# Kernel optimization log

Hardware: AMD Instinct MI355X
Metric: run time of the kernel (lower is better)

Reference implementation:

```python
import jax, jax.numpy as jnp
import numpy as np

DIM = 1024; DEPTH = 2; HEADS = 8; DH = DIM // HEADS  # 128
BUCKET = 64; NHASH = 4; MULT = 4
B = 2; T = 4096
NBUCKETS = T // BUCKET  # 64
SCALE = DH ** -0.5
SELF_ATTN_VAL = -5e4  # TOKEN_SELF_ATTN_VALUE in reformer-pytorch
EPS = 1e-5


def layer_norm(x, g, b):
    m = jnp.mean(x, -1, keepdims=True)
    v = jnp.var(x, -1, keepdims=True)
    return (x - m) * jax.lax.rsqrt(v + EPS) * g + b


def lsh_attn(xn, Wqk, Wv, Wo, bo, rot):
    # xn: [B,T,DIM] already layer-normed. Shared-QK LSH attention (reformer-pytorch).
    qk = (xn @ Wqk).reshape(B, T, HEADS, DH).transpose(0, 2, 1, 3).reshape(B * HEADS, T, DH)
    v = (xn @ Wv).reshape(B, T, HEADS, DH).transpose(0, 2, 1, 3).reshape(B * HEADS, T, DH)
    bh = B * HEADS
    # --- hashing with random rotations ---
    rotated = jnp.einsum('btf,fhi->bhti', qk, rot)            # [bh,NHASH,T,NBUCKETS//2]
    rotated = jnp.concatenate([rotated, -rotated], -1)        # [bh,NHASH,T,NBUCKETS]
    buckets = jnp.argmax(rotated, -1)                         # [bh,NHASH,T]
    offs = (jnp.arange(NHASH) * NBUCKETS)[:, None]
    buckets = (buckets + offs).reshape(bh, NHASH * T)
    ticker = jnp.arange(NHASH * T)
    bt = buckets * T + (ticker % T)                           # unique keys -> stable-equivalent sort
    sticker = jnp.argsort(bt, axis=-1)                        # [bh, NHASH*T]
    undo = jnp.argsort(sticker, axis=-1)
    st = sticker % T                                          # original positions, bucket-sorted
    sqk = jnp.take_along_axis(qk, st[..., None], axis=1)
    sv = jnp.take_along_axis(v, st[..., None], axis=1)
    nchunks = NHASH * NBUCKETS
    bq_t = st.reshape(bh, nchunks, BUCKET)
    bqk = sqk.reshape(bh, nchunks, BUCKET, DH)
    bv = sv.reshape(bh, nchunks, BUCKET, DH)
    bq = bqk
    bk = bqk / jnp.clip(jnp.linalg.norm(bqk, axis=-1, keepdims=True), 1e-12)
    def look_one_back(a):
        extra = jnp.concatenate([a[:, -1:], a[:, :-1]], axis=1)
        return jnp.concatenate([a, extra], axis=2)
    bk = look_one_back(bk); bv = look_one_back(bv); bkv_t = look_one_back(bq_t)
    dots = jnp.einsum('bcie,bcje->bcij', bq, bk) * SCALE      # [bh,nchunks,BUCKET,2*BUCKET]
    self_mask = bq_t[..., :, None] == bkv_t[..., None, :]     # shared-QK: penalize i==j
    dots = jnp.where(self_mask, SELF_ATTN_VAL, dots)
    lse = jax.nn.logsumexp(dots, axis=-1, keepdims=True)
    p = jnp.exp(dots - lse)
    bo_ = jnp.einsum('bcij,bcje->bcie', p, bv)
    so = bo_.reshape(bh, NHASH * T, DH)
    slog = lse.reshape(bh, NHASH * T)
    o = jnp.take_along_axis(so, undo[..., None], axis=1)
    logits = jnp.take_along_axis(slog, undo, axis=1)
    o = o.reshape(bh, NHASH, T, DH)
    logits = logits.reshape(bh, NHASH, T, 1)
    probs = jnp.exp(logits - jax.nn.logsumexp(logits, axis=1, keepdims=True))
    out = jnp.sum(o * probs, axis=1)                          # combine hash rounds
    out = out.reshape(B, HEADS, T, DH).transpose(0, 2, 1, 3).reshape(B, T, HEADS * DH)
    return out @ Wo + bo


def setup_inputs() -> dict:
    key = jax.random.key(0)
    ks = jax.random.split(key, 16)
    s = 0.02
    d = {
        'x': jax.random.normal(ks[0], (B, T, DIM), jnp.float32),
        'ln1_g': jnp.ones((DEPTH, DIM), jnp.float32),
        'ln1_b': jnp.zeros((DEPTH, DIM), jnp.float32),
        'Wqk': jax.random.normal(ks[1], (DEPTH, DIM, HEADS * DH), jnp.float32) * s,
        'Wv': jax.random.normal(ks[2], (DEPTH, DIM, HEADS * DH), jnp.float32) * s,
        'Wo': jax.random.normal(ks[3], (DEPTH, HEADS * DH, DIM), jnp.float32) * s,
        'bo': jnp.zeros((DEPTH, DIM), jnp.float32),
        'ln2_g': jnp.ones((DEPTH, DIM), jnp.float32),
        'ln2_b': jnp.zeros((DEPTH, DIM), jnp.float32),
        'W1': jax.random.normal(ks[4], (DEPTH, DIM, DIM * MULT), jnp.float32) * s,
        'b1': jnp.zeros((DEPTH, DIM * MULT), jnp.float32),
        'W2': jax.random.normal(ks[5], (DEPTH, DIM * MULT, DIM), jnp.float32) * s,
        'b2': jnp.zeros((DEPTH, DIM), jnp.float32),
        'rotations': jax.random.normal(ks[6], (DEPTH, DH, NHASH, NBUCKETS // 2), jnp.float32),
    }
    return d


def reference(x, ln1_g, ln1_b, Wqk, Wv, Wo, bo, ln2_g, ln2_b, W1, b1, W2, b2, rotations):
    xx = jnp.concatenate([x, x], -1)  # [B,T,2*DIM] reversible pair
    def step(carry, p):
        g1, be1, wqk, wv, wo, bov, g2, be2, w1, bb1, w2, bb2, rot = p
        x1, x2 = jnp.split(carry, 2, axis=-1)
        y1 = x1 + lsh_attn(layer_norm(x2, g1, be1), wqk, wv, wo, bov, rot)
        h = layer_norm(y1, g2, be2)
        ff = jax.nn.gelu(h @ w1 + bb1, approximate=False) @ w2 + bb2
        y2 = x2 + ff
        return jnp.concatenate([y1, y2], -1), None
    params = (ln1_g, ln1_b, Wqk, Wv, Wo, bo, ln2_g, ln2_b, W1, b1, W2, b2, rotations)
    out, _ = jax.lax.scan(step, xx, params)
    y1, y2 = jnp.split(out, 2, axis=-1)
    return y1 + y2
```

## Files before the change

### kernel.cpp

```cpp
#include <hip/hip_runtime.h>
#include <hip/hip_bf16.h>
#include <cmath>

using bf16 = __hip_bfloat16;
typedef __attribute__((ext_vector_type(8))) short short8;
typedef __attribute__((ext_vector_type(4))) float floatx4;

__device__ __forceinline__ float bu2f(ushort u) { return __uint_as_float((unsigned)u << 16); }
__device__ __forceinline__ ushort f2bu(float f) {
  union { bf16 b; ushort u; } cv; cv.b = __float2bfloat16(f); return cv.u;
}
__device__ __forceinline__ void gl_lds16(const ushort* g, ushort* l) {
  __builtin_amdgcn_global_load_lds((const __attribute__((address_space(1))) unsigned*)g,
                                   (__attribute__((address_space(3))) unsigned*)l, 16, 0, 0);
}
__device__ __forceinline__ float fast_gelu(float x) {
  float z = 0.7978845608028654f * (x + 0.044715f * x * x * x);
  z = fmaxf(fminf(z, 10.f), -10.f);
  float e = __expf(2.f * z);
  float t = (e - 1.f) / (e + 1.f);
  return 0.5f * x * (1.f + t);
}

static constexpr int kT   = 4096;
static constexpr int kDim = 1024;
static constexpr float kScale   = 0.08838834764831845f;
static constexpr float kSelfVal = -5.0e4f;

__device__ __forceinline__ int sane_v(float f) { float a = fabsf(f); return (a > 1e-4f && a < 1e4f) ? 1 : 0; }

__global__ __launch_bounds__(256) void k_detect(const unsigned* __restrict__ x, int* __restrict__ flag) {
  __shared__ int cnt;
  int tid = threadIdx.x;
  if (tid == 0) cnt = 0;
  __syncthreads();
  int my = 0;
  const uint4* p = (const uint4*)x;
  for (int q = 0; q < 16; q++) {
    uint4 u = p[tid * 16 + q];
    my += sane_v(__uint_as_float(u.x << 16)) + sane_v(__uint_as_float(u.x & 0xffff0000u));
    my += sane_v(__uint_as_float(u.y << 16)) + sane_v(__uint_as_float(u.y & 0xffff0000u));
    my += sane_v(__uint_as_float(u.z << 16)) + sane_v(__uint_as_float(u.z & 0xffff0000u));
    my += sane_v(__uint_as_float(u.w << 16)) + sane_v(__uint_as_float(u.w & 0xffff0000u));
  }
  atomicAdd(&cnt, my);
  __syncthreads();
  if (tid == 0) flag[0] = (cnt >= 24576) ? 1 : 0;
}

__global__ __launch_bounds__(256) void k_cvt(const int* __restrict__ flag, const void* __restrict__ src,
                                             ushort* __restrict__ dst, int n) {
  int i = blockIdx.x * 256 + threadIdx.x;
  if (i >= n) return;
  dst[i] = (*flag) ? ((const ushort*)src)[i] : f2bu(((const float*)src)[i]);
}

__global__ __launch_bounds__(256) void k_init_any(const int* __restrict__ flag, const void* __restrict__ x,
                                                  float* __restrict__ x1, float* __restrict__ x2) {
  int i = blockIdx.x * 1024 + threadIdx.x * 4;
  float4 f;
  if (*flag) {
    ushort4 u = *(const ushort4*)((const ushort*)x + i);
    f.x = bu2f(u.x); f.y = bu2f(u.y); f.z = bu2f(u.z); f.w = bu2f(u.w);
  } else {
    f = *(const float4*)((const float*)x + i);
  }
  *(float4*)(x1 + i) = f;
  *(float4*)(x2 + i) = f;
}

__global__ __launch_bounds__(256) void k_final_any(const int* __restrict__ flag, const float* __restrict__ x1,
                                                   const float* __restrict__ x2, void* __restrict__ out) {
  int i = blockIdx.x * 1024 + threadIdx.x * 4;
  float4 a = *(const float4*)(x1 + i);
  float4 b = *(const float4*)(x2 + i);
  float4 s; s.x = a.x + b.x; s.y = a.y + b.y; s.z = a.z + b.z; s.w = a.w + b.w;
  if (*flag) {
    ushort4 u; u.x = f2bu(s.x); u.y = f2bu(s.y); u.z = f2bu(s.z); u.w = f2bu(s.w);
    *(ushort4*)((ushort*)out + i) = u;
  } else {
    *(float4*)((float*)out + i) = s;
  }
}

__global__ __launch_bounds__(256) void k_ln(const float* __restrict__ x, const ushort* __restrict__ g,
                                            const ushort* __restrict__ be, ushort* __restrict__ out) {
  __shared__ float ws[4], ws2[4];
  int row = blockIdx.x, tid = threadIdx.x;
  const float* xr = x + (size_t)row * kDim + tid * 4;
  float4 v = *(const float4*)xr;
  float s  = v.x + v.y + v.z + v.w;
  float s2 = v.x*v.x + v.y*v.y + v.z*v.z + v.w*v.w;
  #pragma unroll
  for (int off = 32; off; off >>= 1) { s += __shfl_down(s, off); s2 += __shfl_down(s2, off); }
  int wave = tid >> 6, lane = tid & 63;
  if (lane == 0) { ws[wave] = s; ws2[wave] = s2; }
  __syncthreads();
  s  = ws[0] + ws[1] + ws[2] + ws[3];
  s2 = ws2[0] + ws2[1] + ws2[2] + ws2[3];
  float mean = s * (1.f/1024.f);
  float var  = fmaxf(s2 * (1.f/1024.f) - mean*mean, 0.f);
  float rstd = rsqrtf(var + 1e-5f);
  int cb = tid * 4;
  ushort* o = out + (size_t)row * kDim + cb;
  o[0] = f2bu((v.x - mean) * rstd * bu2f(g[cb+0]) + bu2f(be[cb+0]));
  o[1] = f2bu((v.y - mean) * rstd * bu2f(g[cb+1]) + bu2f(be[cb+1]));
  o[2] = f2bu((v.z - mean) * rstd * bu2f(g[cb+2]) + bu2f(be[cb+2]));
  o[3] = f2bu((v.w - mean) * rstd * bu2f(g[cb+3]) + bu2f(be[cb+3]));
}

__global__ __launch_bounds__(256) void k_transpose2(const int* __restrict__ flag, const void* __restrict__ src_bf,
                                                    const void* __restrict__ src_f, ushort* __restrict__ out,
                                                    int K, int N) {
  __shared__ ushort tile[32][33];
  int isbf = *flag;
  int nb = blockIdx.x * 32, kb = blockIdx.y * 32;
  int tx = threadIdx.x & 31, ty = threadIdx.x >> 5;
  for (int r = ty; r < 32; r += 8) {
    size_t idx = (size_t)(kb + r) * N + nb + tx;
    tile[r][tx] = isbf ? ((const ushort*)src_bf)[idx] : f2bu(((const float*)src_f)[idx]);
  }
  __syncthreads();
  for (int r = ty; r < 32; r += 8) out[(size_t)(nb + r) * K + kb + tx] = tile[tx][r];
}

__global__ __launch_bounds__(256) void k_rot_t(const ushort* __restrict__ rot, ushort* __restrict__ rotT) {
  int tid = threadIdx.x;
  for (int idx = tid; idx < 16384; idx += 256) {
    int n = idx >> 7, k = idx & 127;
    rotT[idx] = rot[k * 128 + n];
  }
}

template <int MW>
__global__ __launch_bounds__(512, 2) void k_gemm2(const ushort* __restrict__ A, const ushort* __restrict__ Bt,
                                                  const ushort* __restrict__ bias, float* __restrict__ Cf,
                                                  ushort* __restrict__ Cb, ushort* __restrict__ Cb2,
                                                  int M, int N, int K, int mode) {
  constexpr int BM  = MW * 32;
  constexpr int LA  = MW / 4;
  constexpr int AHI = (MW == 8) ? 4 : 2;
  __shared__ alignas(16) ushort SAu[4 * BM * 32];
  __shared__ alignas(16) ushort SBu[4 * 256 * 32];

  const int tid  = threadIdx.x;
  const int lane = tid & 63, wave = tid >> 6;
  const int lr = lane & 15, g = lane >> 4;
  const int wm = wave >> 2, wn = wave & 3;

  const int nbx = gridDim.x;
  const int nwg = nbx * gridDim.y;
  const int bid = blockIdx.y * nbx + blockIdx.x;
  const int swz = (bid & 7) * (nwg >> 3) + (bid >> 3);
  const int m0 = (swz / nbx) * BM;
  const int n0 = (swz % nbx) * 256;

  const int NT = K >> 5;

  const ushort* srcA[LA];
  #pragma unroll
  for (int j = 0; j < LA; j++) {
    int chunk = wave * (64 * LA) + j * 64 + lane;
    int row = chunk >> 2, c = chunk & 3;
    int cs = c ^ ((row >> 1) & 3);
    srcA[j] = A + (size_t)(m0 + row) * K + cs * 8;
  }
  const ushort* srcB[2];
  #pragma unroll
  for (int j = 0; j < 2; j++) {
    int chunk = wave * 128 + j * 64 + lane;
    int row = chunk >> 2, c = chunk & 3;
    int cs = c ^ ((row >> 1) & 3);
    srcB[j] = Bt + (size_t)(n0 + row) * K + cs * 8;
  }

  int offA[MW], offB[4];
  #pragma unroll
  for (int mi = 0; mi < MW; mi++) {
    int row = wm * (MW * 16) + mi * 16 + lr;
    offA[mi] = row * 32 + ((g ^ ((row >> 1) & 3)) * 8);
  }
  #pragma unroll
  for (int ni = 0; ni < 4; ni++) {
    int row = wn * 64 + ni * 16 + lr;
    offB[ni] = row * 32 + ((g ^ ((row >> 1) & 3)) * 8);
  }

  floatx4 acc[MW][4];
  #pragma unroll
  for (int mi = 0; mi < MW; mi++)
    #pragma unroll
    for (int ni = 0; ni < 4; ni++) acc[mi][ni] = (floatx4){0.f, 0.f, 0.f, 0.f};

  #pragma unroll
  for (int p = 0; p < 3; p++) {
    #pragma unroll
    for (int j = 0; j < LA; j++) gl_lds16(srcA[j] + p * 32, SAu + p * (BM * 32) + (wave * (64 * LA) + j * 64) * 8);
    #pragma unroll
    for (int j = 0; j < 2; j++)  gl_lds16(srcB[j] + p * 32, SBu + p * (256 * 32) + (wave * 128 + j * 64) * 8);
  }
  if constexpr (MW == 8) asm volatile("s_waitcnt vmcnt(8)" ::: "memory");
  else                   asm volatile("s_waitcnt vmcnt(6)" ::: "memory");
  __builtin_amdgcn_s_barrier();
  asm volatile("" ::: "memory");

  for (int kt = 0; kt < NT; kt++) {
    const ushort* sa = SAu + (kt & 3) * (BM * 32);
    const ushort* sb = SBu + (kt & 3) * (256 * 32);
    const bool pf = (kt + 3 < NT);
    const int kp = (kt + 3) * 32, pb = (kt + 3) & 3;

    short8 aA[AHI], bb[4];
    #pragma unroll
    for (int i = 0; i < AHI; i++) aA[i] = *(const short8*)&sa[offA[i]];
    #pragma unroll
    for (int ni = 0; ni < 4; ni++) bb[ni] = *(const short8*)&sb[offB[ni]];
    if (pf) {
      if constexpr (MW == 8) {
        gl_lds16(srcA[0] + kp, SAu + pb * (BM * 32) + (wave * 128 + 0) * 8);
        gl_lds16(srcA[1] + kp, SAu + pb * (BM * 32) + (wave * 128 + 64) * 8);
      } else {
        gl_lds16(srcA[0] + kp, SAu + pb * (BM * 32) + (wave * 64) * 8);
        gl_lds16(srcB[0] + kp, SBu + pb * (256 * 32) + (wave * 128 + 0) * 8);
      }
    }
    __builtin_amdgcn_s_barrier();
    __builtin_amdgcn_sched_barrier(0);
    __builtin_amdgcn_s_setprio(1);
    #pragma unroll
    for (int mi = 0; mi < AHI; mi++)
      #pragma unroll
      for (int ni = 0; ni < 4; ni++)
        acc[mi][ni] = __builtin_amdgcn_mfma_f32_16x16x32_bf16(aA[mi], bb[ni], acc[mi][ni], 0, 0, 0);
    __builtin_amdgcn_s_setprio(0);
    __builtin_amdgcn_sched_barrier(0);
    __builtin_amdgcn_s_barrier();
    asm volatile("" ::: "memory");

    short8 aB[MW - AHI];
    #pragma unroll
    for (int i = 0; i < MW - AHI; i++) aB[i] = *(const short8*)&sa[offA[AHI + i]];
    if (pf) {
      if constexpr (MW == 8) {
        gl_lds16(srcB[0] + kp, SBu + pb * (256 * 32) + (wave * 128 + 0) * 8);
        gl_lds16(srcB[1] + kp, SBu + pb * (256 * 32) + (wave * 128 + 64) * 8);
      } else {
        gl_lds16(srcB[1] + kp, SBu + pb * (256 * 32) + (wave * 128 + 64) * 8);
      }
    }
    if (kt + 3 < NT) {
      if constexpr (MW == 8) asm volatile("s_waitcnt vmcnt(8)" ::: "memory");
      else                   asm volatile("s_waitcnt vmcnt(6)" ::: "memory");
    } else if (kt + 2 < NT) {
      if constexpr (MW == 8) asm volatile("s_waitcnt vmcnt(4)" ::: "memory");
      else                   asm volatile("s_waitcnt vmcnt(3)" ::: "memory");
    } else if (kt + 1 < NT) {
      asm volatile("s_waitcnt vmcnt(0)" ::: "memory");
    }
    __builtin_amdgcn_s_barrier();
    __builtin_amdgcn_sched_barrier(0);
    __builtin_amdgcn_s_setprio(1);
    #pragma unroll
    for (int mi = 0; mi < MW - AHI; mi++)
      #pragma unroll
      for (int ni = 0; ni < 4; ni++)
        acc[AHI + mi][ni] = __builtin_amdgcn_mfma_f32_16x16x32_bf16(aB[mi], bb[ni], acc[AHI + mi][ni], 0, 0, 0);
    __builtin_amdgcn_s_setprio(0);
    __builtin_amdgcn_sched_barrier(0);
    __builtin_amdgcn_s_barrier();
    asm volatile("" ::: "memory");
  }

  const int hi4 = (lane >> 4) * 4;

  if (mode == 1) {
    #pragma unroll
    for (int mi = 0; mi < MW; mi++) {
      #pragma unroll
      for (int ni = 0; ni < 4; ni++) {
        int col = n0 + wn * 64 + ni * 16 + lr;
        float bv = bu2f(bias[col]);
        #pragma unroll
        for (int q = 0; q < 4; q++) {
          int r2 = m0 + wm * (MW * 16) + mi * 16 + hi4 + q;
          Cf[(size_t)r2 * N + col] += acc[mi][ni][q] + bv;
        }
      }
    }
  } else {
    ushort* reg0 = (MW == 8) ? SAu : SBu;
    ushort* reg1 = SBu;
    #pragma unroll
    for (int mi = 0; mi < MW; mi++) {
      #pragma unroll
      for (int ni = 0; ni < 4; ni++) {
        int colw = wn * 64 + ni * 16 + lr;
        float bv = (mode == 2) ? bu2f(bias[n0 + colw]) : 0.f;
        #pragma unroll
        for (int q = 0; q < 4; q++) {
          int grow = wm * (MW * 16) + mi * 16 + hi4 + q;
          ushort* reg = (grow < 128) ? reg0 : reg1;
          int rl = grow & 127;
          float val = acc[mi][ni][q];
          ushort h = (mode == 2) ? f2bu(fast_gelu(val + bv)) : f2bu(val);
          reg[rl * 256 + (((colw >> 3) ^ (rl & 7)) * 8) + (colw & 7)] = h;
        }
      }
    }
    __syncthreads();
    {
      const int j = tid & 31;
      const int rsub = tid >> 5;
      #pragma unroll
      for (int p = 0; p < BM / 16; p++) {
        int row = p * 16 + rsub;
        const ushort* reg = (row < 128) ? reg0 : reg1;
        int rl = row & 127;
        short8 v = *(const short8*)&reg[rl * 256 + ((j ^ (rl & 7)) * 8)];
        *(short8*)&Cb[(size_t)(m0 + row) * N + n0 + j * 8] = v;
      }
    }
    if (mode == 5) {
      __syncthreads();
      #pragma unroll
      for (int mi = 0; mi < MW; mi++) {
        #pragma unroll
        for (int ni = 0; ni < 4; ni++) {
          int colw = wn * 64 + ni * 16 + lr;
          #pragma unroll
          for (int q = 0; q < 4; q++) {
            int grow = wm * (MW * 16) + mi * 16 + hi4 + q;
            ushort* reg = (grow < 128) ? reg0 : reg1;
            int rl = grow & 127;
            float val = acc[mi][ni][q];
            ushort h = f2bu(val);
            reg[rl * 256 + (((colw >> 3) ^ (rl & 7)) * 8) + (colw & 7)] = f2bu(val - bu2f(h));
          }
        }
      }
      __syncthreads();
      const int j = tid & 31;
      const int rsub = tid >> 5;
      #pragma unroll
      for (int p = 0; p < BM / 16; p++) {
        int row = p * 16 + rsub;
        const ushort* reg = (row < 128) ? reg0 : reg1;
        int rl = row & 127;
        short8 v = *(const short8*)&reg[rl * 256 + ((j ^ (rl & 7)) * 8)];
        *(short8*)&Cb2[(size_t)(m0 + row) * N + n0 + j * 8] = v;
      }
    }
  }
  (void)M;
}

__global__ __launch_bounds__(512, 2) void k_gemm3(const ushort* __restrict__ A, const ushort* __restrict__ Bt,
                                                  const ushort* __restrict__ bias, ushort* __restrict__ Cb,
                                                  int M, int N, int K) {
  __shared__ alignas(16) ushort SA[2 * 256 * 64];
  __shared__ alignas(16) ushort SB[2 * 256 * 64];
  const int tid  = threadIdx.x;
  const int lane = tid & 63, wave = tid >> 6;
  const int lr = lane & 15, g = lane >> 4;
  const int wm = wave >> 2, wn = wave & 3;

  const int nbx = gridDim.x;
  const int nwg = nbx * gridDim.y;
  const int bid = blockIdx.y * nbx + blockIdx.x;
  const int swz = (bid & 7) * (nwg >> 3) + (bid >> 3);
  const int m0 = (swz / nbx) * 256;
  const int n0 = (swz % nbx) * 256;
  const int NT = K >> 6;
  const int NI = NT >> 1;

  const int chAr = (wave * 64 + lane) >> 3;
  const int chAs = (wave * 64 + lane) & 7;
  const int swA  = (chAs ^ (chAr & 7)) * 8;
  const ushort* sAq[2][2];
  #pragma unroll
  for (int q = 0; q < 2; q++)
    #pragma unroll
    for (int j = 0; j < 2; j++)
      sAq[q][j] = A + (size_t)(m0 + q * 64 + j * 128 + chAr) * K + swA;
  const int chBr = lane >> 3;
  const int swB  = ((lane & 7) ^ chBr) * 8;
  const ushort* sBh[2][2];
  #pragma unroll
  for (int h = 0; h < 2; h++)
    #pragma unroll
    for (int j = 0; j < 2; j++)
      sBh[h][j] = Bt + (size_t)(n0 + h * 128 + wave * 16 + j * 8 + chBr) * K + swB;

  int rA[8], rB[4], cK[2];
  #pragma unroll
  for (int mi = 0; mi < 8; mi++) rA[mi] = (wm * 128 + mi * 16 + lr) * 64;
  #pragma unroll
  for (int ni = 0; ni < 4; ni++) rB[ni] = (wn * 64 + ni * 16 + lr) * 64;
  cK[0] = ((0 * 4 + g) ^ (lr & 7)) * 8;
  cK[1] = ((1 * 4 + g) ^ (lr & 7)) * 8;

  floatx4 acc[8][4];
  #pragma unroll
  for (int mi = 0; mi < 8; mi++)
    #pragma unroll
    for (int ni = 0; ni < 4; ni++) acc[mi][ni] = (floatx4){0.f, 0.f, 0.f, 0.f};

#define G3_STG_A(d, q, kt) { int ko = ((kt) < NT ? (kt) : 0) << 6; \
    gl_lds16(sAq[q][0] + ko, SA + (d) * 16384 + ((q) * 64 + wave * 8) * 64); \
    gl_lds16(sAq[q][1] + ko, SA + (d) * 16384 + (128 + (q) * 64 + wave * 8) * 64); }
#define G3_STG_B(d, h, kt) { int ko = ((kt) < NT ? (kt) : 0) << 6; \
    gl_lds16(sBh[h][0] + ko, SB + (d) * 16384 + ((h) * 128 + wave * 16) * 64); \
    gl_lds16(sBh[h][1] + ko, SB + (d) * 16384 + ((h) * 128 + wave * 16 + 8) * 64); }
#define G3_RD_A(dst, d, kk, mb) { _Pragma("unroll") \
    for (int _m = 0; _m < 4; _m++) dst[_m] = *(const short8*)&SA[(d) * 16384 + rA[(mb) + _m] + cK[kk]]; }
#define G3_RD_B(dst, d, kk) { _Pragma("unroll") \
    for (int _n = 0; _n < 4; _n++) dst[_n] = *(const short8*)&SB[(d) * 16384 + rB[_n] + cK[kk]]; }
#define G3_MM(mb, af, bf) { \
    __builtin_amdgcn_s_setprio(1); \
    _Pragma("unroll") for (int _m = 0; _m < 4; _m++) \
      _Pragma("unroll") for (int _n = 0; _n < 4; _n++) \
        acc[(mb) + _m][_n] = __builtin_amdgcn_mfma_f32_16x16x32_bf16(af[_m], bf[_n], acc[(mb) + _m][_n], 0, 0, 0); \
    __builtin_amdgcn_s_setprio(0); }
#define G3_BAR()  __builtin_amdgcn_s_barrier()
#define G3_SB()   __builtin_amdgcn_sched_barrier(0)

  G3_STG_A(0, 0, 0); G3_STG_A(0, 1, 0); G3_STG_B(0, 0, 0); G3_STG_B(0, 1, 0);
  G3_STG_A(1, 0, 1); G3_STG_B(1, 0, 1);
  asm volatile("s_waitcnt vmcnt(4)" ::: "memory");
  G3_BAR();
  asm volatile("" ::: "memory");

  for (int i = 0; i < NI; i++) {
    const int kb = 2 * i;
    short8 aA[4], bb0[4], bb1[4];
    G3_RD_A(aA, 0, 0, 0); G3_RD_B(bb0, 0, 0); G3_STG_B(1, 1, kb + 1);
    G3_BAR(); G3_SB();
    G3_MM(0, aA, bb0);
    G3_SB(); G3_BAR(); asm volatile("" ::: "memory");
    G3_RD_A(aA, 0, 1, 0); G3_RD_B(bb1, 0, 1); G3_STG_A(1, 1, kb + 1);
    G3_BAR(); G3_SB();
    G3_MM(0, aA, bb1);
    G3_SB(); G3_BAR(); asm volatile("" ::: "memory");
    G3_RD_A(aA, 0, 0, 4); G3_STG_A(0, 0, kb + 2);
    G3_BAR(); G3_SB();
    G3_MM(4, aA, bb0);
    G3_SB(); G3_BAR(); asm volatile("" ::: "memory");
    G3_RD_A(aA, 0, 1, 4); G3_STG_B(0, 0, kb + 2);
    G3_BAR(); G3_SB();
    G3_MM(4, aA, bb1);
    G3_SB();
    asm volatile("s_waitcnt vmcnt(6)" ::: "memory");
    G3_BAR(); asm volatile("" ::: "memory");
    G3_RD_A(aA, 1, 0, 0); G3_RD_B(bb0, 1, 0); G3_STG_B(0, 1, kb + 2);
    G3_BAR(); G3_SB();
    G3_MM(0, aA, bb0);
    G3_SB(); G3_BAR(); asm volatile("" ::: "memory");
    G3_RD_A(aA, 1, 1, 0); G3_RD_B(bb1, 1, 1); G3_STG_A(0, 1, kb + 2);
    G3_BAR(); G3_SB();
    G3_MM(0, aA, bb1);
    G3_SB();
    asm volatile("s_waitcnt vmcnt(8)" ::: "memory");
    G3_BAR(); asm volatile("" ::: "memory");
    G3_RD_A(aA, 1, 0, 4); G3_STG_A(1, 0, kb + 3);
    G3_BAR(); G3_SB();
    G3_MM(4, aA, bb0);
    G3_SB(); G3_BAR(); asm volatile("" ::: "memory");
    G3_RD_A(aA, 1, 1, 4); G3_STG_B(1, 0, kb + 3);
    G3_BAR(); G3_SB();
    G3_MM(4, aA, bb1);
    G3_SB();
    asm volatile("s_waitcnt vmcnt(4)" ::: "memory");
    G3_BAR(); asm volatile("" ::: "memory");
  }

  asm volatile("s_waitcnt vmcnt(0)" ::: "memory");
  __syncthreads();

  const int hi4 = (lane >> 4) * 4;
  ushort* reg0 = SA;
  ushort* reg1 = SB;
  #pragma unroll
  for (int mi = 0; mi < 8; mi++) {
    #pragma unroll
    for (int ni = 0; ni < 4; ni++) {
      int colw = wn * 64 + ni * 16 + lr;
      float bv = bu2f(bias[n0 + colw]);
      #pragma unroll
      for (int q = 0; q < 4; q++) {
        int grow = wm * 128 + mi * 16 + hi4 + q;
        ushort* reg = (grow < 128) ? reg0 : reg1;
        int rl = grow & 127;
        reg[rl * 256 + (((colw >> 3) ^ (rl & 7)) * 8) + (colw & 7)] = f2bu(fast_gelu(acc[mi][ni][q] + bv));
      }
    }
  }
  __syncthreads();
  {
    const int j = tid & 31;
    const int rsub = tid >> 5;
    #pragma unroll
    for (int p = 0; p < 16; p++) {
      int row = p * 16 + rsub;
      const ushort* reg = (row < 128) ? reg0 : reg1;
      int rl = row & 127;
      short8 v = *(const short8*)&reg[rl * 256 + ((j ^ (rl & 7)) * 8)];
      *(short8*)&Cb[(size_t)(m0 + row) * N + n0 + j * 8] = v;
    }
  }
  (void)M;
#undef G3_STG_A
#undef G3_STG_B
#undef G3_RD_A
#undef G3_RD_B
#undef G3_MM
#undef G3_BAR
#undef G3_SB
}

__global__ __launch_bounds__(256) void k_bucket_mfma(const ushort* __restrict__ qkh, const ushort* __restrict__ qkl,
                                                     const ushort* __restrict__ rotT, int* __restrict__ bkt) {
  __shared__ alignas(16) ushort Bs[128*128];
  __shared__ alignas(16) ushort Ah[64*128];
  __shared__ alignas(16) ushort Al[64*128];
  const int tid = threadIdx.x;
  const int lane = tid & 63, wave = tid >> 6;
  const int lr = lane & 15, lk = (lane >> 4) * 8;
  const int tt = blockIdx.x * 64;
  const int bh = blockIdx.y;
  const int b = bh >> 3, hh = bh & 7;

  {
    int r = tid >> 2, c0 = (tid & 3) * 32;
    size_t base = ((size_t)(b * kT + tt + r)) * kDim + hh * 128 + c0;
    const uint4* sh = (const uint4*)(qkh + base);
    const uint4* sl = (const uint4*)(qkl + base);
    uint4* dh = (uint4*)&Ah[r * 128 + c0];
    uint4* dl = (uint4*)&Al[r * 128 + c0];
    #pragma unroll
    for (int i = 0; i < 4; i++) { dh[i] = sh[i]; dl[i] = sl[i]; }
  }
  {
    const uint4* src = (const uint4*)rotT;
    uint4* dst = (uint4*)Bs;
    for (int i = tid; i < 2048; i += 256) dst[i] = src[i];
  }
  __syncthreads();

  floatx4 acc[4][2];
  #pragma unroll
  for (int mi = 0; mi < 4; mi++) { acc[mi][0] = (floatx4){0,0,0,0}; acc[mi][1] = (floatx4){0,0,0,0}; }
  #pragma unroll
  for (int ks = 0; ks < 4; ks++) {
    short8 a[4], bb[2];
    #pragma unroll
    for (int ni = 0; ni < 2; ni++) bb[ni] = *(const short8*)&Bs[(wave*32 + ni*16 + lr)*128 + ks*32 + lk];
    #pragma unroll
    for (int mi = 0; mi < 4; mi++) a[mi] = *(const short8*)&Ah[(mi*16 + lr)*128 + ks*32 + lk];
    #pragma unroll
    for (int mi = 0; mi < 4; mi++)
      #pragma unroll
      for (int ni = 0; ni < 2; ni++)
        acc[mi][ni] = __builtin_amdgcn_mfma_f32_16x16x32_bf16(a[mi], bb[ni], acc[mi][ni], 0, 0, 0);
  }
  #pragma unroll
  for (int ks = 0; ks < 4; ks++) {
    short8 a[4], bb[2];
    #pragma unroll
    for (int ni = 0; ni < 2; ni++) bb[ni] = *(const short8*)&Bs[(wave*32 + ni*16 + lr)*128 + ks*32 + lk];
    #pragma unroll
    for (int mi = 0; mi < 4; mi++) a[mi] = *(const short8*)&Al[(mi*16 + lr)*128 + ks*32 + lk];
    #pragma unroll
    for (int mi = 0; mi < 4; mi++)
      #pragma unroll
      for (int ni = 0; ni < 2; ni++)
        acc[mi][ni] = __builtin_amdgcn_mfma_f32_16x16x32_bf16(a[mi], bb[ni], acc[mi][ni], 0, 0, 0);
  }

  #pragma unroll
  for (int mi = 0; mi < 4; mi++) {
    #pragma unroll
    for (int q = 0; q < 4; q++) {
      float v0 = acc[mi][0][q];
      float v1 = acc[mi][1][q];
      float best = v0; int bidx = lr;
      if (v1  > best) { best = v1;  bidx = 16 + lr; }
      if (-v0 > best) { best = -v0; bidx = 32 + lr; }
      if (-v1 > best) { best = -v1; bidx = 48 + lr; }
      #pragma unroll
      for (int m = 1; m <= 8; m <<= 1) {
        float ov = __shfl_xor(best, m);
        int   oi = __shfl_xor(bidx, m);
        if (ov > best || (ov == best && oi < bidx)) { best = ov; bidx = oi; }
      }
      if (lr == 0) {
        int row = mi*16 + ((lane >> 4) & 3)*4 + q;
        bkt[(bh*4 + wave)*4096 + tt + row] = bidx;
      }
    }
  }
}

__global__ __launch_bounds__(256) void k_sort(const int* __restrict__ bkt, int* __restrict__ st) {
  __shared__ unsigned char  hist[64*256];
  __shared__ unsigned short offs[64*256];
  __shared__ int base[64];
  int tid = threadIdx.x, grp = blockIdx.x;
  const int* bk = bkt + grp * 4096;
  for (int i = tid; i < 64*256; i += 256) hist[i] = 0;
  __syncthreads();
  int myb[16];
  #pragma unroll
  for (int j = 0; j < 16; j++) {
    myb[j] = bk[tid*16 + j];
    hist[myb[j]*256 + tid] += 1;
  }
  __syncthreads();
  if (tid < 64) {
    int run = 0;
    for (int t = 0; t < 256; t++) { offs[tid*256 + t] = (unsigned short)run; run += hist[tid*256 + t]; }
    base[tid] = run;
  }
  __syncthreads();
  if (tid == 0) {
    int run = 0;
    for (int b2 = 0; b2 < 64; b2++) { int c = base[b2]; base[b2] = run; run += c; }
  }
  __syncthreads();
  #pragma unroll
  for (int j = 0; j < 16; j++) {
    int b2 = myb[j];
    int r = 0;
    for (int jj = 0; jj < j; jj++) r += (myb[jj] == b2) ? 1 : 0;
    st[grp*4096 + base[b2] + (int)offs[b2*256 + tid] + r] = tid*16 + j;
  }
}

__global__ __launch_bounds__(256) void k_attn(const ushort* __restrict__ qkh, const ushort* __restrict__ vbuf,
                                              const int* __restrict__ st, ushort* __restrict__ o_r,
                                              float* __restrict__ lse_r) {
  __shared__ alignas(16) ushort KV[128*136];
  __shared__ alignas(16) ushort Ps[64*136];
  __shared__ float rnorm[128];
  __shared__ int   kposs[128];
  __shared__ float red1[64*4];
  __shared__ float red2[64*4];
  __shared__ float lrow[64];

  const int tid = threadIdx.x;
  const int bid = blockIdx.x;
  const int bh = bid >> 8;
  const int c  = bid & 255;
  const int h  = c >> 6;
  const int cprev = (c + 255) & 255;
  const int b  = bh >> 3, hh = bh & 7;
  const int lane = tid & 63, wave = tid >> 6;
  const int lr = lane & 15, lk = (lane >> 4) * 8;

  {
    int j = tid >> 1, half = tid & 1;
    int slot = (j < 64) ? (c*64 + j) : (cprev*64 + (j - 64));
    int pos = st[bh*16384 + slot];
    if (half == 0) kposs[j] = pos;
    const ushort* src = qkh + ((size_t)(b * kT + pos)) * kDim + hh*128 + half*64;
    float ss = 0.f;
    #pragma unroll
    for (int i2 = 0; i2 < 64; i2 += 8) {
      uint4 u = *(const uint4*)(src + i2);
      *(uint4*)&KV[j*136 + half*64 + i2] = u;
      float f0 = bu2f((ushort)(u.x & 0xffffu)), f1 = bu2f((ushort)(u.x >> 16));
      float f2 = bu2f((ushort)(u.y & 0xffffu)), f3 = bu2f((ushort)(u.y >> 16));
      float f4 = bu2f((ushort)(u.z & 0xffffu)), f5 = bu2f((ushort)(u.z >> 16));
      float f6 = bu2f((ushort)(u.w & 0xffffu)), f7 = bu2f((ushort)(u.w >> 16));
      ss += f0*f0 + f1*f1 + f2*f2 + f3*f3 + f4*f4 + f5*f5 + f6*f6 + f7*f7;
    }
    ss += __shfl_xor(ss, 1);
    if (half == 0) rnorm[j] = 1.f / fmaxf(sqrtf(ss), 1e-12f);
  }
  __syncthreads();

  {
    floatx4 acc[4][2];
    #pragma unroll
    for (int mi = 0; mi < 4; mi++) { acc[mi][0] = (floatx4){0,0,0,0}; acc[mi][1] = (floatx4){0,0,0,0}; }
    #pragma unroll
    for (int ks = 0; ks < 4; ks++) {
      short8 a[4], bb[2];
      #pragma unroll
      for (int mi = 0; mi < 4; mi++) a[mi]  = *(const short8*)&KV[(mi*16 + lr)*136 + ks*32 + lk];
      #pragma unroll
      for (int ni = 0; ni < 2; ni++) bb[ni] = *(const short8*)&KV[(wave*32 + ni*16 + lr)*136 + ks*32 + lk];
      #pragma unroll
      for (int mi = 0; mi < 4; mi++)
        #pragma unroll
        for (int ni = 0; ni < 2; ni++)
          acc[mi][ni] = __builtin_amdgcn_mfma_f32_16x16x32_bf16(a[mi], bb[ni], acc[mi][ni], 0, 0, 0);
    }
    #pragma unroll
    for (int mi = 0; mi < 4; mi++) {
      #pragma unroll
      for (int ni = 0; ni < 2; ni++) {
        int col = wave*32 + ni*16 + lr;
        float rn = rnorm[col] * kScale;
        int cpos = kposs[col];
        #pragma unroll
        for (int q = 0; q < 4; q++) {
          int row = mi*16 + (lane >> 4)*4 + q;
          float val = acc[mi][ni][q] * rn;
          if (cpos == kposs[row]) val = kSelfVal;
          Ps[row*136 + col] = f2bu(val);
        }
      }
    }
  }
  __syncthreads();

  {
    int j = tid >> 1, half = tid & 1;
    int pos = kposs[j];
    const ushort* src = vbuf + ((size_t)(b * kT + pos)) * kDim + hh*128 + half*64;
    #pragma unroll
    for (int i2 = 0; i2 < 64; i2 += 8) {
      uint4 u = *(const uint4*)(src + i2);
      int d0 = half*64 + i2;
      KV[(d0+0)*136 + j] = (ushort)(u.x & 0xffffu); KV[(d0+1)*136 + j] = (ushort)(u.x >> 16);
      KV[(d0+2)*136 + j] = (ushort)(u.y & 0xffffu); KV[(d0+3)*136 + j] = (ushort)(u.y >> 16);
      KV[(d0+4)*136 + j] = (ushort)(u.z & 0xffffu); KV[(d0+5)*136 + j] = (ushort)(u.z >> 16);
      KV[(d0+6)*136 + j] = (ushort)(u.w & 0xffffu); KV[(d0+7)*136 + j] = (ushort)(u.w >> 16);
    }
  }

  {
    int i = tid >> 2, part = tid & 3;
    const int jb = part * 32;
    float m = -1e30f;
    for (int j2 = 0; j2 < 32; j2++) m = fmaxf(m, bu2f(Ps[i*136 + jb + j2]));
    red1[i*4 + part] = m;
    __syncthreads();
    m = fmaxf(fmaxf(red1[i*4+0], red1[i*4+1]), fmaxf(red1[i*4+2], red1[i*4+3]));
    float ssum = 0.f;
    for (int j2 = 0; j2 < 32; j2++) {
      float arg = fmaxf(fminf(bu2f(Ps[i*136 + jb + j2]) - m, 0.f), -80.f);
      float p = __expf(arg);
      ssum += p;
      Ps[i*136 + jb + j2] = f2bu(p);
    }
    red2[i*4 + part] = ssum;
    __syncthreads();
    if (part == 0) {
      float l = fmaxf(red2[i*4+0] + red2[i*4+1] + red2[i*4+2] + red2[i*4+3], 1e-20f);
      lrow[i] = 1.f / l;
      lse_r[(size_t)(bh*4 + h)*4096 + kposs[i]] = m + __logf(l);
    }
  }
  __syncthreads();

  {
    floatx4 acc[4][2];
    #pragma unroll
    for (int mi = 0; mi < 4; mi++) { acc[mi][0] = (floatx4){0,0,0,0}; acc[mi][1] = (floatx4){0,0,0,0}; }
    #pragma unroll
    for (int ks = 0; ks < 4; ks++) {
      short8 a[4], bb[2];
      #pragma unroll
      for (int mi = 0; mi < 4; mi++) a[mi]  = *(const short8*)&Ps[(mi*16 + lr)*136 + ks*32 + lk];
      #pragma unroll
      for (int ni = 0; ni < 2; ni++) bb[ni] = *(const short8*)&KV[(wave*32 + ni*16 + lr)*136 + ks*32 + lk];
      #pragma unroll
      for (int mi = 0; mi < 4; mi++)
        #pragma unroll
        for (int ni = 0; ni < 2; ni++)
          acc[mi][ni] = __builtin_amdgcn_mfma_f32_16x16x32_bf16(a[mi], bb[ni], acc[mi][ni], 0, 0, 0);
    }
    #pragma unroll
    for (int mi = 0; mi < 4; mi++) {
      #pragma unroll
      for (int ni = 0; ni < 2; ni++) {
        int d = wave*32 + ni*16 + lr;
        #pragma unroll
        for (int q = 0; q < 4; q++) {
          int row = mi*16 + (lane >> 4)*4 + q;
          float o = acc[mi][ni][q] * lrow[row];
          o_r[((size_t)(bh*4 + h)*4096 + kposs[row])*128 + d] = f2bu(o);
        }
      }
    }
  }
}

__global__ __launch_bounds__(256) void k_combine(const ushort* __restrict__ o_r, const float* __restrict__ lse_r,
                                                 ushort* __restrict__ attnbf) {
  int rid = blockIdx.x * 2 + (threadIdx.x >> 7);
  int d = threadIdx.x & 127;
  int bh = rid >> 12, t = rid & 4095;
  int b = bh >> 3, hh = bh & 7;
  size_t base = (size_t)bh * 16384 + t;
  float l0 = lse_r[base], l1 = lse_r[base + 4096], l2 = lse_r[base + 8192], l3 = lse_r[base + 12288];
  float M = fmaxf(fmaxf(l0, l1), fmaxf(l2, l3));
  float e0 = __expf(fmaxf(fminf(l0 - M, 0.f), -80.f));
  float e1 = __expf(fmaxf(fminf(l1 - M, 0.f), -80.f));
  float e2 = __expf(fmaxf(fminf(l2 - M, 0.f), -80.f));
  float e3 = __expf(fmaxf(fminf(l3 - M, 0.f), -80.f));
  float inv = 1.f / (e0 + e1 + e2 + e3);
  float o = e0 * bu2f(o_r[(base         )*128 + d]) + e1 * bu2f(o_r[(base +  4096)*128 + d])
          + e2 * bu2f(o_r[(base +  8192)*128 + d]) + e3 * bu2f(o_r[(base + 12288)*128 + d]);
  attnbf[((size_t)b * kT + t) * kDim + hh*128 + d] = f2bu(o * inv);
}

extern "C" void kernel_launch(void* const* d_in, const int* in_sizes, int n_in,
                              void* d_out, int out_size, void* d_ws, size_t ws_size,
                              hipStream_t stream) {
  (void)in_sizes; (void)n_in; (void)out_size; (void)ws_size;
  const void* x     = d_in[0];
  const void* ln1_g = d_in[1];
  const void* ln1_b = d_in[2];
  const void* Wqk   = d_in[3];
  const void* Wv    = d_in[4];
  const void* Wo    = d_in[5];
  const void* bo    = d_in[6];
  const void* ln2_g = d_in[7];
  const void* ln2_b = d_in[8];
  const void* W1    = d_in[9];
  const void* b1    = d_in[10];
  const void* W2    = d_in[11];
  const void* b2    = d_in[12];
  const void* rot   = d_in[13];

  char* w = (char*)d_ws;
  int*    flag = (int*)w;    w += 256;
  ushort* prm  = (ushort*)w; w += 131072;
  float* x1  = (float*)w;  w += 33554432;
  float* x2  = (float*)w;  w += 33554432;
  ushort* qkh = (ushort*)w; w += 16777216;
  ushort* qkl = (ushort*)w; w += 16777216;
  ushort* vbb = (ushort*)w; w += 16777216;
  ushort* xbf = (ushort*)w; w += 16777216;
  ushort* orb = (ushort*)w; w += 67108864;
  float* lse = (float*)w;  w += 1048576;
  int*   bkt = (int*)w;    w += 1048576;
  int*   stb = (int*)w;    w += 1048576;
  ushort* wtA = (ushort*)w; w += 2097152;
  ushort* wtB = (ushort*)w; w += 2097152;
  ushort* wtC = (ushort*)w; w += 2097152;
  ushort* wt1 = (ushort*)w; w += 8388608;
  ushort* wt2 = (ushort*)w; w += 8388608;
  ushort* rtT = (ushort*)w; w += 32768;

  ushort* pLN1G = prm + 0;     ushort* pLN1B = prm + 2048;
  ushort* pBO   = prm + 4096;  ushort* pLN2G = prm + 6144;
  ushort* pLN2B = prm + 8192;  ushort* pB1   = prm + 10240;
  ushort* pB2   = prm + 18432; ushort* pROT  = prm + 20480;

  k_detect<<<1, 256, 0, stream>>>((const unsigned*)x, flag);
  k_cvt<<<8,   256, 0, stream>>>(flag, ln1_g, pLN1G, 2048);
  k_cvt<<<8,   256, 0, stream>>>(flag, ln1_b, pLN1B, 2048);
  k_cvt<<<8,   256, 0, stream>>>(flag, bo,    pBO,   2048);
  k_cvt<<<8,   256, 0, stream>>>(flag, ln2_g, pLN2G, 2048);
  k_cvt<<<8,   256, 0, stream>>>(flag, ln2_b, pLN2B, 2048);
  k_cvt<<<32,  256, 0, stream>>>(flag, b1,    pB1,   8192);
  k_cvt<<<8,   256, 0, stream>>>(flag, b2,    pB2,   2048);
  k_cvt<<<128, 256, 0, stream>>>(flag, rot,   pROT,  32768);
  k_init_any<<<8192, 256, 0, stream>>>(flag, x, x1, x2);

  for (int d = 0; d < 2; d++) {
    k_transpose2<<<dim3(32, 32),  256, 0, stream>>>(flag,
        (const char*)Wqk + (size_t)d*1048576*2, (const char*)Wqk + (size_t)d*1048576*4, wtA, 1024, 1024);
    k_transpose2<<<dim3(32, 32),  256, 0, stream>>>(flag,
        (const char*)Wv  + (size_t)d*1048576*2, (const char*)Wv  + (size_t)d*1048576*4, wtB, 1024, 1024);
    k_transpose2<<<dim3(32, 32),  256, 0, stream>>>(flag,
        (const char*)Wo  + (size_t)d*1048576*2, (const char*)Wo  + (size_t)d*1048576*4, wtC, 1024, 1024);
    k_transpose2<<<dim3(128, 32), 256, 0, stream>>>(flag,
        (const char*)W1  + (size_t)d*4194304*2, (const char*)W1  + (size_t)d*4194304*4, wt1, 1024, 4096);
    k_transpose2<<<dim3(32, 128), 256, 0, stream>>>(flag,
        (const char*)W2  + (size_t)d*4194304*2, (const char*)W2  + (size_t)d*4194304*4, wt2, 4096, 1024);
    k_rot_t<<<1, 256, 0, stream>>>(pROT + (size_t)d * 16384, rtT);

    k_ln<<<8192, 256, 0, stream>>>(x2, pLN1G + d*1024, pLN1B + d*1024, xbf);
    k_gemm2<4><<<dim3(4, 64), 512, 0, stream>>>(xbf, wtA, nullptr, nullptr, qkh, qkl, 8192, 1024, 1024, 5);
    k_gemm2<4><<<dim3(4, 64), 512, 0, stream>>>(xbf, wtB, nullptr, nullptr, vbb, nullptr, 8192, 1024, 1024, 3);
    k_bucket_mfma<<<dim3(64, 16), 256, 0, stream>>>(qkh, qkl, rtT, bkt);
    k_sort<<<64, 256, 0, stream>>>(bkt, stb);
    k_attn<<<4096, 256, 0, stream>>>(qkh, vbb, stb, orb, lse);
    k_combine<<<32768, 256, 0, stream>>>(orb, lse, xbf);
    k_gemm2<4><<<dim3(4, 64), 512, 0, stream>>>(xbf, wtC, pBO + d*1024, x1, nullptr, nullptr, 8192, 1024, 1024, 1);
    k_ln<<<8192, 256, 0, stream>>>(x1, pLN2G + d*1024, pLN2B + d*1024, xbf);
    k_gemm3<<<dim3(16, 32), 512, 0, stream>>>(xbf, wt1, pB1 + d*4096, orb, 8192, 4096, 1024);
    k_gemm2<4><<<dim3(4, 64), 512, 0, stream>>>(orb, wt2, pB2 + d*1024, x2, nullptr, nullptr, 8192, 1024, 4096, 1);
  }
  k_final_any<<<8192, 256, 0, stream>>>(flag, x1, x2, d_out);
}
```

Measured before the change: 1.170 ms.

## Replace N=1024 GEMM with K=64 triple-buffered pipeline kernel

```diff
diff --git a/kernel.cpp b/kernel.cpp
--- a/kernel.cpp
+++ b/kernel.cpp
@@ -132,17 +132,12 @@
   }
 }
 
-template <int MW>
-__global__ __launch_bounds__(512, 2) void k_gemm2(const ushort* __restrict__ A, const ushort* __restrict__ Bt,
+__global__ __launch_bounds__(512, 2) void k_gemm4(const ushort* __restrict__ A, const ushort* __restrict__ Bt,
                                                   const ushort* __restrict__ bias, float* __restrict__ Cf,
                                                   ushort* __restrict__ Cb, ushort* __restrict__ Cb2,
                                                   int M, int N, int K, int mode) {
-  constexpr int BM  = MW * 32;
-  constexpr int LA  = MW / 4;
-  constexpr int AHI = (MW == 8) ? 4 : 2;
-  __shared__ alignas(16) ushort SAu[4 * BM * 32];
-  __shared__ alignas(16) ushort SBu[4 * 256 * 32];
-
+  __shared__ alignas(16) ushort SA[3 * 128 * 64];
+  __shared__ alignas(16) ushort SB[3 * 256 * 64];
   const int tid  = threadIdx.x;
   const int lane = tid & 63, wave = tid >> 6;
   const int lr = lane & 15, g = lane >> 4;
@@ -152,158 +147,120 @@
   const int nwg = nbx * gridDim.y;
   const int bid = blockIdx.y * nbx + blockIdx.x;
   const int swz = (bid & 7) * (nwg >> 3) + (bid >> 3);
-  const int m0 = (swz / nbx) * BM;
+  const int m0 = (swz / nbx) * 128;
   const int n0 = (swz % nbx) * 256;
-
-  const int NT = K >> 5;
-
-  const ushort* srcA[LA];
-  #pragma unroll
-  for (int j = 0; j < LA; j++) {
-    int chunk = wave * (64 * LA) + j * 64 + lane;
-    int row = chunk >> 2, c = chunk & 3;
-    int cs = c ^ ((row >> 1) & 3);
-    srcA[j] = A + (size_t)(m0 + row) * K + cs * 8;
-  }
-  const ushort* srcB[2];
-  #pragma unroll
-  for (int j = 0; j < 2; j++) {
-    int chunk = wave * 128 + j * 64 + lane;
-    int row = chunk >> 2, c = chunk & 3;
-    int cs = c ^ ((row >> 1) & 3);
-    srcB[j] = Bt + (size_t)(n0 + row) * K + cs * 8;
-  }
-
-  int offA[MW], offB[4];
-  #pragma unroll
-  for (int mi = 0; mi < MW; mi++) {
-    int row = wm * (MW * 16) + mi * 16 + lr;
-    offA[mi] = row * 32 + ((g ^ ((row >> 1) & 3)) * 8);
-  }
-  #pragma unroll
-  for (int ni = 0; ni < 4; ni++) {
-    int row = wn * 64 + ni * 16 + lr;
-    offB[ni] = row * 32 + ((g ^ ((row >> 1) & 3)) * 8);
-  }
-
-  floatx4 acc[MW][4];
-  #pragma unroll
-  for (int mi = 0; mi < MW; mi++)
+  const int NT = K >> 6;
+
+  const int srow = (wave * 64 + lane) >> 3;
+  const int sc   = ((lane & 7) ^ (srow & 7)) * 8;
+  const ushort* sA[2];
+  #pragma unroll
+  for (int j = 0; j < 2; j++) sA[j] = A + (size_t)(m0 + j * 64 + srow) * K + sc;
+  const ushort* sB[4];
+  #pragma unroll
+  for (int h = 0; h < 4; h++) sB[h] = Bt + (size_t)(n0 + h * 64 + srow) * K + sc;
+
+  int rA[4], rB[4], cK[2];
+  #pragma unroll
+  for (int mi = 0; mi < 4; mi++) rA[mi] = (wm * 64 + mi * 16 + lr) * 64;
+  #pragma unroll
+  for (int ni = 0; ni < 4; ni++) rB[ni] = (wn * 64 + ni * 16 + lr) * 64;
+  cK[0] = ((0 * 4 + g) ^ (lr & 7)) * 8;
+  cK[1] = ((1 * 4 + g) ^ (lr & 7)) * 8;
+
+  floatx4 acc[4][4];
+  #pragma unroll
+  for (int mi = 0; mi < 4; mi++)
     #pragma unroll
     for (int ni = 0; ni < 4; ni++) acc[mi][ni] = (floatx4){0.f, 0.f, 0.f, 0.f};
 
-  #pragma unroll
-  for (int p = 0; p < 3; p++) {
-    #pragma unroll
-    for (int j = 0; j < LA; j++) gl_lds16(srcA[j] + p * 32, SAu + p * (BM * 32) + (wave * (64 * LA) + j * 64) * 8);
-    #pragma unroll
-    for (int j = 0; j < 2; j++)  gl_lds16(srcB[j] + p * 32, SBu + p * (256 * 32) + (wave * 128 + j * 64) * 8);
-  }
-  if constexpr (MW == 8) asm volatile("s_waitcnt vmcnt(8)" ::: "memory");
-  else                   asm volatile("s_waitcnt vmcnt(6)" ::: "memory");
-  __builtin_amdgcn_s_barrier();
+#define G4_STG_A(bf, j, ko) gl_lds16(sA[j] + (ko), SA + (bf) * 8192  + ((j) * 64 + wave * 8) * 64)
+#define G4_STG_B(bf, h, ko) gl_lds16(sB[h] + (ko), SB + (bf) * 16384 + ((h) * 64 + wave * 8) * 64)
+#define G4_BAR()  __builtin_amdgcn_s_barrier()
+#define G4_SB()   __builtin_amdgcn_sched_barrier(0)
+
+  #pragma unroll
+  for (int p = 0; p < 2; p++) {
+    const int ko = p << 6;
+    G4_STG_A(p, 0, ko); G4_STG_A(p, 1, ko);
+    G4_STG_B(p, 0, ko); G4_STG_B(p, 1, ko); G4_STG_B(p, 2, ko); G4_STG_B(p, 3, ko);
+  }
+  asm volatile("s_waitcnt vmcnt(6)" ::: "memory");
+  G4_BAR();
   asm volatile("" ::: "memory");
 
   for (int kt = 0; kt < NT; kt++) {
-    const ushort* sa = SAu + (kt & 3) * (BM * 32);
-    const ushort* sb = SBu + (kt & 3) * (256 * 32);
-    const bool pf = (kt + 3 < NT);
-    const int kp = (kt + 3) * 32, pb = (kt + 3) & 3;
-
-    short8 aA[AHI], bb[4];
-    #pragma unroll
-    for (int i = 0; i < AHI; i++) aA[i] = *(const short8*)&sa[offA[i]];
-    #pragma unroll
-    for (int ni = 0; ni < 4; ni++) bb[ni] = *(const short8*)&sb[offB[ni]];
-    if (pf) {
-      if constexpr (MW == 8) {
-        gl_lds16(srcA[0] + kp, SAu + pb * (BM * 32) + (wave * 128 + 0) * 8);
-        gl_lds16(srcA[1] + kp, SAu + pb * (BM * 32) + (wave * 128 + 64) * 8);
-      } else {
-        gl_lds16(srcA[0] + kp, SAu + pb * (BM * 32) + (wave * 64) * 8);
-        gl_lds16(srcB[0] + kp, SBu + pb * (256 * 32) + (wave * 128 + 0) * 8);
-      }
-    }
-    __builtin_amdgcn_s_barrier();
-    __builtin_amdgcn_sched_barrier(0);
+    const int cur = kt % 3;
+    const int pb  = (kt + 2) % 3;
+    const int ko  = (kt + 2 < NT) ? ((kt + 2) << 6) : 0;
+    const ushort* sa = SA + cur * 8192;
+    const ushort* sb = SB + cur * 16384;
+    short8 av[4], bv[4];
+
+    #pragma unroll
+    for (int mi = 0; mi < 4; mi++) av[mi] = *(const short8*)&sa[rA[mi] + cK[0]];
+    #pragma unroll
+    for (int ni = 0; ni < 4; ni++) bv[ni] = *(const short8*)&sb[rB[ni] + cK[0]];
+    G4_STG_A(pb, 0, ko); G4_STG_A(pb, 1, ko); G4_STG_B(pb, 0, ko);
+    G4_BAR(); G4_SB();
     __builtin_amdgcn_s_setprio(1);
     #pragma unroll
-    for (int mi = 0; mi < AHI; mi++)
+    for (int mi = 0; mi < 4; mi++)
       #pragma unroll
       for (int ni = 0; ni < 4; ni++)
-        acc[mi][ni] = __builtin_amdgcn_mfma_f32_16x16x32_bf16(aA[mi], bb[ni], acc[mi][ni], 0, 0, 0);
+        acc[mi][ni] = __builtin_amdgcn_mfma_f32_16x16x32_bf16(av[mi], bv[ni], acc[mi][ni], 0, 0, 0);
     __builtin_amdgcn_s_setprio(0);
-    __builtin_amdgcn_sched_barrier(0);
-    __builtin_amdgcn_s_barrier();
+    G4_SB(); G4_BAR();
     asm volatile("" ::: "memory");
 
-    short8 aB[MW - AHI];
-    #pragma unroll
-    for (int i = 0; i < MW - AHI; i++) aB[i] = *(const short8*)&sa[offA[AHI + i]];
-    if (pf) {
-      if constexpr (MW == 8) {
-        gl_lds16(srcB[0] + kp, SBu + pb * (256 * 32) + (wave * 128 + 0) * 8);
-        gl_lds16(srcB[1] + kp, SBu + pb * (256 * 32) + (wave * 128 + 64) * 8);
-      } else {
-        gl_lds16(srcB[1] + kp, SBu + pb * (256 * 32) + (wave * 128 + 64) * 8);
-      }
-    }
-    if (kt + 3 < NT) {
-      if constexpr (MW == 8) asm volatile("s_waitcnt vmcnt(8)" ::: "memory");
-      else                   asm volatile("s_waitcnt vmcnt(6)" ::: "memory");
-    } else if (kt + 2 < NT) {
-      if constexpr (MW == 8) asm volatile("s_waitcnt vmcnt(4)" ::: "memory");
-      else                   asm volatile("s_waitcnt vmcnt(3)" ::: "memory");
-    } else if (kt + 1 < NT) {
-      asm volatile("s_waitcnt vmcnt(0)" ::: "memory");
-    }
-    __builtin_amdgcn_s_barrier();
-    __builtin_amdgcn_sched_barrier(0);
+    #pragma unroll
+    for (int mi = 0; mi < 4; mi++) av[mi] = *(const short8*)&sa[rA[mi] + cK[1]];
+    #pragma unroll
+    for (int ni = 0; ni < 4; ni++) bv[ni] = *(const short8*)&sb[rB[ni] + cK[1]];
+    G4_STG_B(pb, 1, ko); G4_STG_B(pb, 2, ko); G4_STG_B(pb, 3, ko);
+    G4_BAR(); G4_SB();
     __builtin_amdgcn_s_setprio(1);
     #pragma unroll
-    for (int mi = 0; mi < MW - AHI; mi++)
+    for (int mi = 0; mi < 4; mi++)
       #pragma unroll
       for (int ni = 0; ni < 4; ni++)
-        acc[AHI + mi][ni] = __builtin_amdgcn_mfma_f32_16x16x32_bf16(aB[mi], bb[ni], acc[AHI + mi][ni], 0, 0, 0);
+        acc[mi][ni] = __builtin_amdgcn_mfma_f32_16x16x32_bf16(av[mi], bv[ni], acc[mi][ni], 0, 0, 0);
     __builtin_amdgcn_s_setprio(0);
-    __builtin_amdgcn_sched_barrier(0);
-    __builtin_amdgcn_s_barrier();
+    G4_SB();
+    asm volatile("s_waitcnt vmcnt(6)" ::: "memory");
+    G4_BAR();
     asm volatile("" ::: "memory");
   }
 
+  asm volatile("s_waitcnt vmcnt(0)" ::: "memory");
+  __syncthreads();
+
   const int hi4 = (lane >> 4) * 4;
 
   if (mode == 1) {
     #pragma unroll
-    for (int mi = 0; mi < MW; mi++) {
+    for (int mi = 0; mi < 4; mi++) {
       #pragma unroll
       for (int ni = 0; ni < 4; ni++) {
         int col = n0 + wn * 64 + ni * 16 + lr;
-        float bv = bu2f(bias[col]);
+        float bv2 = bu2f(bias[col]);
         #pragma unroll
         for (int q = 0; q < 4; q++) {
-          int r2 = m0 + wm * (MW * 16) + mi * 16 + hi4 + q;
-          Cf[(size_t)r2 * N + col] += acc[mi][ni][q] + bv;
+          int r2 = m0 + wm * 64 + mi * 16 + hi4 + q;
+          Cf[(size_t)r2 * N + col] += acc[mi][ni][q] + bv2;
         }
       }
     }
   } else {
-    ushort* reg0 = (MW == 8) ? SAu : SBu;
-    ushort* reg1 = SBu;
-    #pragma unroll
-    for (int mi = 0; mi < MW; mi++) {
+    #pragma unroll
+    for (int mi = 0; mi < 4; mi++) {
       #pragma unroll
       for (int ni = 0; ni < 4; ni++) {
         int colw = wn * 64 + ni * 16 + lr;
-        float bv = (mode == 2) ? bu2f(bias[n0 + colw]) : 0.f;
         #pragma unroll
         for (int q = 0; q < 4; q++) {
-          int grow = wm * (MW * 16) + mi * 16 + hi4 + q;
-          ushort* reg = (grow < 128) ? reg0 : reg1;
-          int rl = grow & 127;
-          float val = acc[mi][ni][q];
-          ushort h = (mode == 2) ? f2bu(fast_gelu(val + bv)) : f2bu(val);
-          reg[rl * 256 + (((colw >> 3) ^ (rl & 7)) * 8) + (colw & 7)] = h;
+          int grow = wm * 64 + mi * 16 + hi4 + q;
+          SB[grow * 256 + (((colw >> 3) ^ (grow & 7)) * 8) + (colw & 7)] = f2bu(acc[mi][ni][q]);
         }
       }
     }
@@ -312,29 +269,25 @@
       const int j = tid & 31;
       const int rsub = tid >> 5;
       #pragma unroll
-      for (int p = 0; p < BM / 16; p++) {
+      for (int p = 0; p < 8; p++) {
         int row = p * 16 + rsub;
-        const ushort* reg = (row < 128) ? reg0 : reg1;
-        int rl = row & 127;
-        short8 v = *(const short8*)&reg[rl * 256 + ((j ^ (rl & 7)) * 8)];
+        short8 v = *(const short8*)&SB[row * 256 + ((j ^ (row & 7)) * 8)];
         *(short8*)&Cb[(size_t)(m0 + row) * N + n0 + j * 8] = v;
       }
     }
     if (mode == 5) {
       __syncthreads();
       #pragma unroll
-      for (int mi = 0; mi < MW; mi++) {
+      for (int mi = 0; mi < 4; mi++) {
         #pragma unroll
         for (int ni = 0; ni < 4; ni++) {
           int colw = wn * 64 + ni * 16 + lr;
           #pragma unroll
           for (int q = 0; q < 4; q++) {
-            int grow = wm * (MW * 16) + mi * 16 + hi4 + q;
-            ushort* reg = (grow < 128) ? reg0 : reg1;
-            int rl = grow & 127;
+            int grow = wm * 64 + mi * 16 + hi4 + q;
             float val = acc[mi][ni][q];
             ushort h = f2bu(val);
-            reg[rl * 256 + (((colw >> 3) ^ (rl & 7)) * 8) + (colw & 7)] = f2bu(val - bu2f(h));
+            SB[grow * 256 + (((colw >> 3) ^ (grow & 7)) * 8) + (colw & 7)] = f2bu(val - bu2f(h));
           }
         }
       }
@@ -342,16 +295,18 @@
       const int j = tid & 31;
       const int rsub = tid >> 5;
       #pragma unroll
-      for (int p = 0; p < BM / 16; p++) {
+      for (int p = 0; p < 8; p++) {
         int row = p * 16 + rsub;
-        const ushort* reg = (row < 128) ? reg0 : reg1;
-        int rl = row & 127;
-        short8 v = *(const short8*)&reg[rl * 256 + ((j ^ (rl & 7)) * 8)];
+        short8 v = *(const short8*)&SB[row * 256 + ((j ^ (row & 7)) * 8)];
         *(short8*)&Cb2[(size_t)(m0 + row) * N + n0 + j * 8] = v;
       }
     }
   }
   (void)M;
+#undef G4_STG_A
+#undef G4_STG_B
+#undef G4_BAR
+#undef G4_SB
 }
 
 __global__ __launch_bounds__(512, 2) void k_gemm3(const ushort* __restrict__ A, const ushort* __restrict__ Bt,
@@ -875,16 +830,16 @@
     k_rot_t<<<1, 256, 0, stream>>>(pROT + (size_t)d * 16384, rtT);
 
     k_ln<<<8192, 256, 0, stream>>>(x2, pLN1G + d*1024, pLN1B + d*1024, xbf);
-    k_gemm2<4><<<dim3(4, 64), 512, 0, stream>>>(xbf, wtA, nullptr, nullptr, qkh, qkl, 8192, 1024, 1024, 5);
-    k_gemm2<4><<<dim3(4, 64), 512, 0, stream>>>(xbf, wtB, nullptr, nullptr, vbb, nullptr, 8192, 1024, 1024, 3);
+    k_gemm4<<<dim3(4, 64), 512, 0, stream>>>(xbf, wtA, nullptr, nullptr, qkh, qkl, 8192, 1024, 1024, 5);
+    k_gemm4<<<dim3(4, 64), 512, 0, stream>>>(xbf, wtB, nullptr, nullptr, vbb, nullptr, 8192, 1024, 1024, 3);
     k_bucket_mfma<<<dim3(64, 16), 256, 0, stream>>>(qkh, qkl, rtT, bkt);
     k_sort<<<64, 256, 0, stream>>>(bkt, stb);
     k_attn<<<4096, 256, 0, stream>>>(qkh, vbb, stb, orb, lse);
     k_combine<<<32768, 256, 0, stream>>>(orb, lse, xbf);
-    k_gemm2<4><<<dim3(4, 64), 512, 0, stream>>>(xbf, wtC, pBO + d*1024, x1, nullptr, nullptr, 8192, 1024, 1024, 1);
+    k_gemm4<<<dim3(4, 64), 512, 0, stream>>>(xbf, wtC, pBO + d*1024, x1, nullptr, nullptr, 8192, 1024, 1024, 1);
     k_ln<<<8192, 256, 0, stream>>>(x1, pLN2G + d*1024, pLN2B + d*1024, xbf);
     k_gemm3<<<dim3(16, 32), 512, 0, stream>>>(xbf, wt1, pB1 + d*4096, orb, 8192, 4096, 1024);
-    k_gemm2<4><<<dim3(4, 64), 512, 0, stream>>>(orb, wt2, pB2 + d*1024, x2, nullptr, nullptr, 8192, 1024, 4096, 1);
+    k_gemm4<<<dim3(4, 64), 512, 0, stream>>>(orb, wt2, pB2 + d*1024, x2, nullptr, nullptr, 8192, 1024, 4096, 1);
   }
   k_final_any<<<8192, 256, 0, stream>>>(flag, x1, x2, d_out);
 }
```

Result: faster. 1.111 ms (-5.1%).
